# Kernel optimization log

Measured on AMD Instinct MI355X. Metric: run time of the kernel, lower is better.

## Reference

```python
import jax, jax.numpy as jnp
import numpy as np
import math

B, S, D, H = 4, 2048, 768, 12
DK = D // H

def setup_inputs() -> dict:
    key = jax.random.key(0)
    ks = jax.random.split(key, 12)
    sc = 1.0 / math.sqrt(D)
    return {
        'Q': jax.random.normal(ks[0], (B, S, D), jnp.float32),
        'K': jax.random.normal(ks[1], (B, S, D), jnp.float32),
        'V': jax.random.normal(ks[2], (B, S, D), jnp.float32),
        'mask': jax.random.randint(ks[3], (B, 1, S, S), 0, 2, jnp.int32),
        'Wq': jax.random.normal(ks[4], (D, D), jnp.float32) * sc,
        'bq': jnp.zeros((D,), jnp.float32),
        'Wk': jax.random.normal(ks[5], (D, D), jnp.float32) * sc,
        'bk': jnp.zeros((D,), jnp.float32),
        'Wv': jax.random.normal(ks[6], (D, D), jnp.float32) * sc,
        'bv': jnp.zeros((D,), jnp.float32),
        'Wo': jax.random.normal(ks[7], (D, D), jnp.float32) * sc,
        'bo': jnp.zeros((D,), jnp.float32),
    }

def _split_heads(x):
    # [B,S,D] -> [B,H,S,DK]
    return x.reshape(B, S, H, DK).transpose(0, 2, 1, 3)

def reference(Q, K, V, mask, Wq, bq, Wk, bk, Wv, bv, Wo, bo):
    q = _split_heads(Q @ Wq.T + bq)
    k = _split_heads(K @ Wk.T + bk)
    v = _split_heads(V @ Wv.T + bv)
    scores = jnp.einsum('bhqd,bhkd->bhqk', q, k) / math.sqrt(DK)
    # Faithful to the source: masked positions are filled with -1e-9 (NOT -inf)
    scores = jnp.where(mask == 0, jnp.float32(-1e-9), scores)
    attn = jax.nn.softmax(scores, axis=-1)
    x = jnp.einsum('bhqk,bhkd->bhqd', attn, v)          # [B,H,S,DK]
    x = x.transpose(0, 2, 1, 3).reshape(B, S, D)         # [B,S,D]
    return x @ Wo.T + bo
```

## Files before the change

kernel.cpp:

```cpp
#include <hip/hip_runtime.h>

#define BB 4
#define SS 2048
#define DD 768
#define HH 12
#define DKK 64
#define MM (BB*SS)

typedef __attribute__((ext_vector_type(8))) short bf16x8;
typedef __attribute__((ext_vector_type(4))) float f32x4;

#define GLDS(g, l) __builtin_amdgcn_global_load_lds( \
    (const __attribute__((address_space(1))) unsigned int*)(g), \
    (__attribute__((address_space(3))) unsigned int*)(l), 16, 0, 0)

__device__ __forceinline__ unsigned short f2bf(float f) {
    union { float f; unsigned int u; } v; v.f = f;
    unsigned int r = v.u + 0x7fffu + ((v.u >> 16) & 1u);
    return (unsigned short)(r >> 16);
}

__global__ void cvt_bf16(const float* __restrict__ src, unsigned short* __restrict__ dst, int n4) {
    int i = blockIdx.x * blockDim.x + threadIdx.x;
    if (i >= n4) return;
    float4 v = ((const float4*)src)[i];
    ushort4 o;
    o.x = f2bf(v.x); o.y = f2bf(v.y); o.z = f2bf(v.z); o.w = f2bf(v.w);
    ((ushort4*)dst)[i] = o;
}

__global__ void mask_pack(const int* __restrict__ mask, unsigned int* __restrict__ mbits) {
    int t = blockIdx.x * blockDim.x + threadIdx.x;
    int m = mask[t];
    unsigned long long b = __ballot(m != 0);
    int l = t & 63;
    if (l == 0)       mbits[t >> 5] = (unsigned int)b;
    else if (l == 32) mbits[t >> 5] = (unsigned int)(b >> 32);
}

__global__ __launch_bounds__(256) void gemm_qkv(
    const unsigned short* __restrict__ Qc, const unsigned short* __restrict__ Kc, const unsigned short* __restrict__ Vc,
    const unsigned short* __restrict__ Wq, const unsigned short* __restrict__ Wk, const unsigned short* __restrict__ Wv,
    const float* __restrict__ bq, const float* __restrict__ bk, const float* __restrict__ bv,
    unsigned short* __restrict__ qb, unsigned short* __restrict__ kb, unsigned short* __restrict__ vt)
{
    __shared__ unsigned short As[128*32];
    __shared__ unsigned short Bs[128*32];
    const int mat = blockIdx.z;
    const unsigned short* X = mat == 0 ? Qc : mat == 1 ? Kc : Vc;
    const unsigned short* W = mat == 0 ? Wq : mat == 1 ? Wk : Wv;
    const float* bias        = mat == 0 ? bq : mat == 1 ? bk : bv;

    const int tid  = threadIdx.x;
    const int lane = tid & 63;
    const int w    = tid >> 6;
    const int wm   = w >> 1, wn = w & 1;
    const int quad = lane >> 4, c = lane & 15;
    const int m0 = blockIdx.y * 128, n0 = blockIdx.x * 128;

    f32x4 acc[4][4];
    #pragma unroll
    for (int i = 0; i < 4; i++)
        #pragma unroll
        for (int j = 0; j < 4; j++) acc[i][j] = (f32x4){0.f, 0.f, 0.f, 0.f};

    const int ch0 = tid, ch1 = 256 + tid;
    const int r0 = ch0 >> 2, cc0 = (ch0 & 3) << 3;
    const int r1 = ch1 >> 2, cc1 = (ch1 & 3) << 3;
    const unsigned short* Xg0 = X + (size_t)(m0 + r0) * DD + cc0;
    const unsigned short* Xg1 = X + (size_t)(m0 + r1) * DD + cc1;
    const unsigned short* Wg0 = W + (size_t)(n0 + r0) * DD + cc0;
    const unsigned short* Wg1 = W + (size_t)(n0 + r1) * DD + cc1;

    for (int k0 = 0; k0 < DD; k0 += 32) {
        GLDS(Xg0 + k0, As + ch0 * 8);
        GLDS(Xg1 + k0, As + ch1 * 8);
        GLDS(Wg0 + k0, Bs + ch0 * 8);
        GLDS(Wg1 + k0, Bs + ch1 * 8);
        __syncthreads();
        bf16x8 a[4], b[4];
        #pragma unroll
        for (int t = 0; t < 4; t++) {
            a[t] = *(const bf16x8*)(As + ((wm * 64 + t * 16 + c) * 32 + quad * 8));
            b[t] = *(const bf16x8*)(Bs + ((wn * 64 + t * 16 + c) * 32 + quad * 8));
        }
        #pragma unroll
        for (int tm = 0; tm < 4; tm++)
            #pragma unroll
            for (int tn = 0; tn < 4; tn++)
                acc[tm][tn] = __builtin_amdgcn_mfma_f32_16x16x32_bf16(a[tm], b[tn], acc[tm][tn], 0, 0, 0);
        __syncthreads();
    }

    if (mat < 2) {
        unsigned short* out = mat == 0 ? qb : kb;
        #pragma unroll
        for (int tn = 0; tn < 4; tn++) {
            const int col = n0 + wn * 64 + tn * 16 + c;
            const float bz = bias[col];
            #pragma unroll
            for (int tm = 0; tm < 4; tm++) {
                const int row = m0 + wm * 64 + tm * 16 + quad * 4;
                #pragma unroll
                for (int r = 0; r < 4; r++)
                    out[(size_t)(row + r) * DD + col] = f2bf(acc[tm][tn][r] + bz);
            }
        }
    } else {
        #pragma unroll
        for (int tn = 0; tn < 4; tn++) {
            const int col = n0 + wn * 64 + tn * 16 + c;
            const float bz = bias[col];
            const int h = col >> 6, dk = col & 63;
            #pragma unroll
            for (int tm = 0; tm < 4; tm++) {
                const int row = m0 + wm * 64 + tm * 16 + quad * 4;
                const int bb = row >> 11, s = row & 2047;
                ushort4 pk;
                pk.x = f2bf(acc[tm][tn][0] + bz);
                pk.y = f2bf(acc[tm][tn][1] + bz);
                pk.z = f2bf(acc[tm][tn][2] + bz);
                pk.w = f2bf(acc[tm][tn][3] + bz);
                *(ushort4*)(vt + ((((size_t)bb * HH + h) * DKK + dk) * SS + s)) = pk;
            }
        }
    }
}

#define EXPSCALE 0.18033688011112042f

__global__ __launch_bounds__(256, 6) void flash(
    const unsigned short* __restrict__ qb, const unsigned short* __restrict__ kb,
    const unsigned short* __restrict__ vt, const unsigned int* __restrict__ mbits,
    unsigned short* __restrict__ ob)
{
    __shared__ unsigned short Ks[2][64*32];
    __shared__ unsigned short Vs[2][64*32];
    __shared__ unsigned short Pb[4][16][72];

    const int bh = blockIdx.y;
    const int bi = bh / HH, h = bh % HH;
    const int tid  = threadIdx.x;
    const int w    = tid >> 6, lane = tid & 63;
    const int quad = lane >> 4, c = lane & 15;
    const int q0 = blockIdx.x * 64 + w * 16;

    const unsigned short* qbase = qb + (size_t)(bi * SS + q0 + c) * DD + h * DKK + quad * 8;
    const bf16x8 qa0 = *(const bf16x8*)(qbase);
    const bf16x8 qa1 = *(const bf16x8*)(qbase + 32);

    const int sr = tid >> 2, sc8 = (tid & 3) << 3;
    const unsigned short* kg0 = kb + ((size_t)bi * SS + sr) * DD + h * DKK + sc8;
    const unsigned short* vg0 = vt + (((size_t)bi * HH + h) * DKK + sr) * SS + sc8;
    unsigned short* lk0 = Ks[0] + tid * 8;
    unsigned short* lk1 = Ks[1] + tid * 8;
    unsigned short* lv0 = Vs[0] + tid * 8;
    unsigned short* lv1 = Vs[1] + tid * 8;

    const unsigned int* mrow = mbits + (size_t)(bi * SS + q0 + c) * (SS / 32);

    f32x4 o[4];
    #pragma unroll
    for (int i = 0; i < 4; i++) o[i] = (f32x4){0.f, 0.f, 0.f, 0.f};
    float rs = 0.f;

    for (int k0 = 0; k0 < SS; k0 += 64) {
        const unsigned short* kg = kg0 + (size_t)k0 * DD;
        const unsigned short* vg = vg0 + k0;
        GLDS(kg,      lk0);
        GLDS(kg + 32, lk1);
        GLDS(vg,      lv0);
        GLDS(vg + 32, lv1);
        __syncthreads();

        const uint2 mw = *(const uint2*)(mrow + (k0 >> 5));
        const unsigned long long mm =
            (((unsigned long long)mw.y << 32) | mw.x) >> (quad * 4);

        #pragma unroll
        for (int nt = 0; nt < 4; nt++) {
            const bf16x8 kf0 = *(const bf16x8*)(Ks[0] + (nt * 16 + c) * 32 + quad * 8);
            const bf16x8 kf1 = *(const bf16x8*)(Ks[1] + (nt * 16 + c) * 32 + quad * 8);
            f32x4 st = (f32x4){0.f, 0.f, 0.f, 0.f};
            st = __builtin_amdgcn_mfma_f32_16x16x32_bf16(kf0, qa0, st, 0, 0, 0);
            st = __builtin_amdgcn_mfma_f32_16x16x32_bf16(kf1, qa1, st, 0, 0, 0);
            const unsigned int mb = (unsigned int)(mm >> (nt * 16));
            unsigned int pk[2];
            #pragma unroll
            for (int r2 = 0; r2 < 2; r2++) {
                float sv0 = st[r2 * 2]     * EXPSCALE;
                float sv1 = st[r2 * 2 + 1] * EXPSCALE;
                sv0 = (mb & (1u << (r2 * 2)))     ? sv0 : 0.0f;
                sv1 = (mb & (1u << (r2 * 2 + 1))) ? sv1 : 0.0f;
                const float p0 = __builtin_amdgcn_exp2f(sv0);
                const float p1 = __builtin_amdgcn_exp2f(sv1);
                rs += p0 + p1;
                union { float f; unsigned int u; } u0, u1; u0.f = p0; u1.f = p1;
                pk[r2] = __builtin_amdgcn_perm(u1.u + 0x8000u, u0.u + 0x8000u, 0x07060302);
            }
            *(uint2*)(&Pb[w][c][nt * 16 + quad * 4]) = make_uint2(pk[0], pk[1]);
        }

        const bf16x8 pa0 = *(const bf16x8*)(&Pb[w][c][quad * 8]);
        const bf16x8 pa1 = *(const bf16x8*)(&Pb[w][c][32 + quad * 8]);
        #pragma unroll
        for (int nt = 0; nt < 4; nt++) {
            const bf16x8 vf0 = *(const bf16x8*)(Vs[0] + (nt * 16 + c) * 32 + quad * 8);
            const bf16x8 vf1 = *(const bf16x8*)(Vs[1] + (nt * 16 + c) * 32 + quad * 8);
            o[nt] = __builtin_amdgcn_mfma_f32_16x16x32_bf16(pa0, vf0, o[nt], 0, 0, 0);
            o[nt] = __builtin_amdgcn_mfma_f32_16x16x32_bf16(pa1, vf1, o[nt], 0, 0, 0);
        }
        __syncthreads();
    }

    rs += __shfl_xor(rs, 16);
    rs += __shfl_xor(rs, 32);
    const float rn = __builtin_amdgcn_rcpf(rs);
    float rr[4];
    #pragma unroll
    for (int reg = 0; reg < 4; reg++)
        rr[reg] = __shfl(rn, quad * 4 + reg, 64);

    unsigned short* op = ob + (size_t)(bi * SS + q0 + quad * 4) * DD + h * DKK + c;
    #pragma unroll
    for (int nt = 0; nt < 4; nt++)
        #pragma unroll
        for (int reg = 0; reg < 4; reg++)
            op[(size_t)reg * DD + nt * 16] = f2bf(o[nt][reg] * rr[reg]);
}

__global__ __launch_bounds__(256) void gemm_out(
    const unsigned short* __restrict__ A, const unsigned short* __restrict__ W,
    const float* __restrict__ bias, float* __restrict__ out)
{
    __shared__ unsigned short As[128*32];
    __shared__ unsigned short Bs[128*32];
    const int tid  = threadIdx.x;
    const int lane = tid & 63;
    const int w    = tid >> 6;
    const int wm   = w >> 1, wn = w & 1;
    const int quad = lane >> 4, c = lane & 15;
    const int m0 = blockIdx.y * 128, n0 = blockIdx.x * 128;

    f32x4 acc[4][4];
    #pragma unroll
    for (int i = 0; i < 4; i++)
        #pragma unroll
        for (int j = 0; j < 4; j++) acc[i][j] = (f32x4){0.f, 0.f, 0.f, 0.f};

    const int ch0 = tid, ch1 = 256 + tid;
    const int r0 = ch0 >> 2, cc0 = (ch0 & 3) << 3;
    const int r1 = ch1 >> 2, cc1 = (ch1 & 3) << 3;
    const unsigned short* Ag0 = A + (size_t)(m0 + r0) * DD + cc0;
    const unsigned short* Ag1 = A + (size_t)(m0 + r1) * DD + cc1;
    const unsigned short* Wg0 = W + (size_t)(n0 + r0) * DD + cc0;
    const unsigned short* Wg1 = W + (size_t)(n0 + r1) * DD + cc1;

    for (int k0 = 0; k0 < DD; k0 += 32) {
        GLDS(Ag0 + k0, As + ch0 * 8);
        GLDS(Ag1 + k0, As + ch1 * 8);
        GLDS(Wg0 + k0, Bs + ch0 * 8);
        GLDS(Wg1 + k0, Bs + ch1 * 8);
        __syncthreads();
        bf16x8 a[4], b[4];
        #pragma unroll
        for (int t = 0; t < 4; t++) {
            a[t] = *(const bf16x8*)(As + ((wm * 64 + t * 16 + c) * 32 + quad * 8));
            b[t] = *(const bf16x8*)(Bs + ((wn * 64 + t * 16 + c) * 32 + quad * 8));
        }
        #pragma unroll
        for (int tm = 0; tm < 4; tm++)
            #pragma unroll
            for (int tn = 0; tn < 4; tn++)
                acc[tm][tn] = __builtin_amdgcn_mfma_f32_16x16x32_bf16(a[tm], b[tn], acc[tm][tn], 0, 0, 0);
        __syncthreads();
    }

    #pragma unroll
    for (int tn = 0; tn < 4; tn++) {
        const int col = n0 + wn * 64 + tn * 16 + c;
        const float bz = bias[col];
        #pragma unroll
        for (int tm = 0; tm < 4; tm++) {
            const int row = m0 + wm * 64 + tm * 16 + quad * 4;
            #pragma unroll
            for (int r = 0; r < 4; r++)
                out[(size_t)(row + r) * DD + col] = acc[tm][tn][r] + bz;
        }
    }
}

extern "C" void kernel_launch(void* const* d_in, const int* in_sizes, int n_in,
                              void* d_out, int out_size, void* d_ws, size_t ws_size,
                              hipStream_t stream) {
    (void)in_sizes; (void)n_in; (void)out_size; (void)ws_size;
    const float* Q    = (const float*)d_in[0];
    const float* K    = (const float*)d_in[1];
    const float* V    = (const float*)d_in[2];
    const int*   mask = (const int*)d_in[3];
    const float* Wq   = (const float*)d_in[4];
    const float* bq   = (const float*)d_in[5];
    const float* Wk   = (const float*)d_in[6];
    const float* bk   = (const float*)d_in[7];
    const float* Wv   = (const float*)d_in[8];
    const float* bv   = (const float*)d_in[9];
    const float* Wo   = (const float*)d_in[10];
    const float* bo   = (const float*)d_in[11];
    float* out = (float*)d_out;

    char* ws = (char*)d_ws;
    size_t off = 0;
    auto alloc = [&](size_t bytes) { char* p = ws + off; off += (bytes + 255) & ~255ULL; return p; };
    const size_t act = (size_t)MM * DD * 2;
    unsigned short* Qc  = (unsigned short*)alloc(act);
    unsigned short* Kc  = (unsigned short*)alloc(act);
    unsigned short* Vc  = (unsigned short*)alloc(act);
    unsigned short* Wqc = (unsigned short*)alloc((size_t)DD * DD * 2);
    unsigned short* Wkc = (unsigned short*)alloc((size_t)DD * DD * 2);
    unsigned short* Wvc = (unsigned short*)alloc((size_t)DD * DD * 2);
    unsigned short* Woc = (unsigned short*)alloc((size_t)DD * DD * 2);
    unsigned short* qb  = (unsigned short*)alloc(act);
    unsigned short* kb  = (unsigned short*)alloc(act);
    unsigned short* vt  = (unsigned short*)alloc(act);
    unsigned int*  mbits = (unsigned int*)alloc((size_t)BB * SS * (SS / 32) * 4);
    unsigned short* ob = Qc;

    const int nact4 = MM * DD / 4;
    const int nw4   = DD * DD / 4;
    cvt_bf16<<<dim3(nact4 / 256), 256, 0, stream>>>(Q, Qc, nact4);
    cvt_bf16<<<dim3(nact4 / 256), 256, 0, stream>>>(K, Kc, nact4);
    cvt_bf16<<<dim3(nact4 / 256), 256, 0, stream>>>(V, Vc, nact4);
    cvt_bf16<<<dim3(nw4 / 256),   256, 0, stream>>>(Wq, Wqc, nw4);
    cvt_bf16<<<dim3(nw4 / 256),   256, 0, stream>>>(Wk, Wkc, nw4);
    cvt_bf16<<<dim3(nw4 / 256),   256, 0, stream>>>(Wv, Wvc, nw4);
    cvt_bf16<<<dim3(nw4 / 256),   256, 0, stream>>>(Wo, Woc, nw4);
    mask_pack<<<dim3(BB * SS * SS / 256), 256, 0, stream>>>(mask, mbits);
    gemm_qkv<<<dim3(DD / 128, MM / 128, 3), 256, 0, stream>>>(
        Qc, Kc, Vc, Wqc, Wkc, Wvc, bq, bk, bv, qb, kb, vt);
    flash<<<dim3(SS / 64, BB * HH), 256, 0, stream>>>(qb, kb, vt, mbits, ob);
    gemm_out<<<dim3(DD / 128, MM / 128), 256, 0, stream>>>(ob, Woc, bo, out);
}
```

Before: 389.8 us.

## Fuse prep kernels, double-buffer and swizzle flash tiles, two query tiles per wave

The eight conversion and mask-packing launches become one prep kernel, which removes launch overhead. The flash kernel now handles 128 queries per block, two 16-row tiles per wave, so each K/V tile in LDS is reused twice. It also double-buffers the K/V loads so the next tile is fetched during compute, dropping one barrier per iteration, and XOR-swizzles the LDS columns to avoid bank conflicts. In exchange it uses more registers and LDS (occupancy hint lowered from 6 to 3) and launches half as many flash blocks.

After: 374.0 us. -4.0%, faster.

```diff
diff --git a/kernel.cpp b/kernel.cpp
--- a/kernel.cpp
+++ b/kernel.cpp
@@ -20,22 +20,48 @@
     return (unsigned short)(r >> 16);
 }
 
-__global__ void cvt_bf16(const float* __restrict__ src, unsigned short* __restrict__ dst, int n4) {
-    int i = blockIdx.x * blockDim.x + threadIdx.x;
-    if (i >= n4) return;
-    float4 v = ((const float4*)src)[i];
-    ushort4 o;
-    o.x = f2bf(v.x); o.y = f2bf(v.y); o.z = f2bf(v.z); o.w = f2bf(v.w);
-    ((ushort4*)dst)[i] = o;
-}
-
-__global__ void mask_pack(const int* __restrict__ mask, unsigned int* __restrict__ mbits) {
-    int t = blockIdx.x * blockDim.x + threadIdx.x;
-    int m = mask[t];
-    unsigned long long b = __ballot(m != 0);
-    int l = t & 63;
-    if (l == 0)       mbits[t >> 5] = (unsigned int)b;
-    else if (l == 32) mbits[t >> 5] = (unsigned int)(b >> 32);
+#define NACT4 (MM*DD/4)
+#define ABLK  (NACT4/256)
+#define NW4   (DD*DD/4)
+#define WBLK  (NW4/256)
+#define MBLK  (BB*SS*SS/256)
+
+__global__ void prep(
+    const float* __restrict__ Q, const float* __restrict__ K, const float* __restrict__ V,
+    const float* __restrict__ Wq, const float* __restrict__ Wk, const float* __restrict__ Wv,
+    const float* __restrict__ Wo, const int* __restrict__ mask,
+    unsigned short* __restrict__ Qc, unsigned short* __restrict__ Kc, unsigned short* __restrict__ Vc,
+    unsigned short* __restrict__ Wqc, unsigned short* __restrict__ Wkc, unsigned short* __restrict__ Wvc,
+    unsigned short* __restrict__ Woc, unsigned int* __restrict__ mbits)
+{
+    const int bx = blockIdx.x;
+    if (bx < 3 * ABLK) {
+        const int seg = bx / ABLK;
+        const float* s = seg == 0 ? Q : seg == 1 ? K : V;
+        unsigned short* d = seg == 0 ? Qc : seg == 1 ? Kc : Vc;
+        const int i = (bx - seg * ABLK) * 256 + threadIdx.x;
+        float4 v = ((const float4*)s)[i];
+        ushort4 o;
+        o.x = f2bf(v.x); o.y = f2bf(v.y); o.z = f2bf(v.z); o.w = f2bf(v.w);
+        ((ushort4*)d)[i] = o;
+    } else if (bx < 3 * ABLK + 4 * WBLK) {
+        const int b2 = bx - 3 * ABLK;
+        const int seg = b2 / WBLK;
+        const float* s = seg == 0 ? Wq : seg == 1 ? Wk : seg == 2 ? Wv : Wo;
+        unsigned short* d = seg == 0 ? Wqc : seg == 1 ? Wkc : seg == 2 ? Wvc : Woc;
+        const int i = (b2 - seg * WBLK) * 256 + threadIdx.x;
+        float4 v = ((const float4*)s)[i];
+        ushort4 o;
+        o.x = f2bf(v.x); o.y = f2bf(v.y); o.z = f2bf(v.z); o.w = f2bf(v.w);
+        ((ushort4*)d)[i] = o;
+    } else {
+        const int t = (bx - (3 * ABLK + 4 * WBLK)) * 256 + threadIdx.x;
+        const int m = mask[t];
+        unsigned long long b = __ballot(m != 0);
+        const int l = t & 63;
+        if (l == 0)       mbits[t >> 5] = (unsigned int)b;
+        else if (l == 32) mbits[t >> 5] = (unsigned int)(b >> 32);
+    }
 }
 
 __global__ __launch_bounds__(256) void gemm_qkv(
@@ -129,104 +155,140 @@
 
 #define EXPSCALE 0.18033688011112042f
 
-__global__ __launch_bounds__(256, 6) void flash(
+__global__ __launch_bounds__(256, 3) void flash(
     const unsigned short* __restrict__ qb, const unsigned short* __restrict__ kb,
     const unsigned short* __restrict__ vt, const unsigned int* __restrict__ mbits,
     unsigned short* __restrict__ ob)
 {
-    __shared__ unsigned short Ks[2][64*32];
-    __shared__ unsigned short Vs[2][64*32];
-    __shared__ unsigned short Pb[4][16][72];
+    __shared__ unsigned short Ks[2][2][64*32];
+    __shared__ unsigned short Vs[2][2][64*32];
+    __shared__ unsigned short Pb[4][32][72];
 
     const int bh = blockIdx.y;
     const int bi = bh / HH, h = bh % HH;
     const int tid  = threadIdx.x;
     const int w    = tid >> 6, lane = tid & 63;
     const int quad = lane >> 4, c = lane & 15;
-    const int q0 = blockIdx.x * 64 + w * 16;
-
-    const unsigned short* qbase = qb + (size_t)(bi * SS + q0 + c) * DD + h * DKK + quad * 8;
-    const bf16x8 qa0 = *(const bf16x8*)(qbase);
-    const bf16x8 qa1 = *(const bf16x8*)(qbase + 32);
-
-    const int sr = tid >> 2, sc8 = (tid & 3) << 3;
-    const unsigned short* kg0 = kb + ((size_t)bi * SS + sr) * DD + h * DKK + sc8;
-    const unsigned short* vg0 = vt + (((size_t)bi * HH + h) * DKK + sr) * SS + sc8;
-    unsigned short* lk0 = Ks[0] + tid * 8;
-    unsigned short* lk1 = Ks[1] + tid * 8;
-    unsigned short* lv0 = Vs[0] + tid * 8;
-    unsigned short* lv1 = Vs[1] + tid * 8;
-
-    const unsigned int* mrow = mbits + (size_t)(bi * SS + q0 + c) * (SS / 32);
-
-    f32x4 o[4];
-    #pragma unroll
-    for (int i = 0; i < 4; i++) o[i] = (f32x4){0.f, 0.f, 0.f, 0.f};
-    float rs = 0.f;
-
-    for (int k0 = 0; k0 < SS; k0 += 64) {
-        const unsigned short* kg = kg0 + (size_t)k0 * DD;
-        const unsigned short* vg = vg0 + k0;
-        GLDS(kg,      lk0);
-        GLDS(kg + 32, lk1);
-        GLDS(vg,      lv0);
-        GLDS(vg + 32, lv1);
-        __syncthreads();
-
-        const uint2 mw = *(const uint2*)(mrow + (k0 >> 5));
-        const unsigned long long mm =
-            (((unsigned long long)mw.y << 32) | mw.x) >> (quad * 4);
+    const int q0w = blockIdx.x * 128 + w * 32;
+
+    bf16x8 qa[2][2];
+    #pragma unroll
+    for (int mt = 0; mt < 2; mt++) {
+        const unsigned short* qbase = qb + (size_t)(bi * SS + q0w + mt * 16 + c) * DD + h * DKK + quad * 8;
+        qa[mt][0] = *(const bf16x8*)(qbase);
+        qa[mt][1] = *(const bf16x8*)(qbase + 32);
+    }
+
+    const int sr = tid >> 2, slot = tid & 3;
+    const int lc = ((slot ^ (sr & 3)) << 3);
+    const unsigned short* kgb = kb + ((size_t)bi * SS + sr) * DD + h * DKK + lc;
+    const unsigned short* vgb = vt + (((size_t)bi * HH + h) * DKK + sr) * SS + lc;
+    unsigned short* lds_k0[2] = { Ks[0][0] + tid * 8, Ks[1][0] + tid * 8 };
+    unsigned short* lds_k1[2] = { Ks[0][1] + tid * 8, Ks[1][1] + tid * 8 };
+    unsigned short* lds_v0[2] = { Vs[0][0] + tid * 8, Vs[1][0] + tid * 8 };
+    unsigned short* lds_v1[2] = { Vs[0][1] + tid * 8, Vs[1][1] + tid * 8 };
+
+    const unsigned int* mrow0 = mbits + (size_t)(bi * SS + q0w + c) * (SS / 32);
+    const unsigned int* mrow1 = mrow0 + (size_t)16 * (SS / 32);
+
+    f32x4 o[2][4];
+    #pragma unroll
+    for (int mt = 0; mt < 2; mt++)
+        #pragma unroll
+        for (int nt = 0; nt < 4; nt++) o[mt][nt] = (f32x4){0.f, 0.f, 0.f, 0.f};
+    float rs[2] = {0.f, 0.f};
+
+    const int sw = ((quad ^ (c & 3)) << 3);
+
+    GLDS(kgb,      lds_k0[0]);
+    GLDS(kgb + 32, lds_k1[0]);
+    GLDS(vgb,      lds_v0[0]);
+    GLDS(vgb + 32, lds_v1[0]);
+
+    for (int t = 0; t < SS / 64; t++) {
+        const int k0 = t * 64, par = t & 1;
+        __syncthreads();
+        if (t < SS / 64 - 1) {
+            const unsigned short* kg = kgb + (size_t)(k0 + 64) * DD;
+            const unsigned short* vg = vgb + (k0 + 64);
+            GLDS(kg,      lds_k0[par ^ 1]);
+            GLDS(kg + 32, lds_k1[par ^ 1]);
+            GLDS(vg,      lds_v0[par ^ 1]);
+            GLDS(vg + 32, lds_v1[par ^ 1]);
+        }
+
+        const uint2 mw0 = *(const uint2*)(mrow0 + (k0 >> 5));
+        const uint2 mw1 = *(const uint2*)(mrow1 + (k0 >> 5));
+        const unsigned long long mm[2] = {
+            ((((unsigned long long)mw0.y << 32) | mw0.x) >> (quad * 4)),
+            ((((unsigned long long)mw1.y << 32) | mw1.x) >> (quad * 4)) };
 
         #pragma unroll
         for (int nt = 0; nt < 4; nt++) {
-            const bf16x8 kf0 = *(const bf16x8*)(Ks[0] + (nt * 16 + c) * 32 + quad * 8);
-            const bf16x8 kf1 = *(const bf16x8*)(Ks[1] + (nt * 16 + c) * 32 + quad * 8);
-            f32x4 st = (f32x4){0.f, 0.f, 0.f, 0.f};
-            st = __builtin_amdgcn_mfma_f32_16x16x32_bf16(kf0, qa0, st, 0, 0, 0);
-            st = __builtin_amdgcn_mfma_f32_16x16x32_bf16(kf1, qa1, st, 0, 0, 0);
-            const unsigned int mb = (unsigned int)(mm >> (nt * 16));
-            unsigned int pk[2];
-            #pragma unroll
-            for (int r2 = 0; r2 < 2; r2++) {
-                float sv0 = st[r2 * 2]     * EXPSCALE;
-                float sv1 = st[r2 * 2 + 1] * EXPSCALE;
-                sv0 = (mb & (1u << (r2 * 2)))     ? sv0 : 0.0f;
-                sv1 = (mb & (1u << (r2 * 2 + 1))) ? sv1 : 0.0f;
-                const float p0 = __builtin_amdgcn_exp2f(sv0);
-                const float p1 = __builtin_amdgcn_exp2f(sv1);
-                rs += p0 + p1;
-                union { float f; unsigned int u; } u0, u1; u0.f = p0; u1.f = p1;
-                pk[r2] = __builtin_amdgcn_perm(u1.u + 0x8000u, u0.u + 0x8000u, 0x07060302);
+            const bf16x8 kf0 = *(const bf16x8*)(&Ks[par][0][(nt * 16 + c) * 32 + sw]);
+            const bf16x8 kf1 = *(const bf16x8*)(&Ks[par][1][(nt * 16 + c) * 32 + sw]);
+            #pragma unroll
+            for (int mt = 0; mt < 2; mt++) {
+                f32x4 st = (f32x4){0.f, 0.f, 0.f, 0.f};
+                st = __builtin_amdgcn_mfma_f32_16x16x32_bf16(kf0, qa[mt][0], st, 0, 0, 0);
+                st = __builtin_amdgcn_mfma_f32_16x16x32_bf16(kf1, qa[mt][1], st, 0, 0, 0);
+                const unsigned int mb = (unsigned int)(mm[mt] >> (nt * 16));
+                unsigned int pk[2];
+                #pragma unroll
+                for (int r2 = 0; r2 < 2; r2++) {
+                    float sv0 = st[r2 * 2]     * EXPSCALE;
+                    float sv1 = st[r2 * 2 + 1] * EXPSCALE;
+                    sv0 = (mb & (1u << (r2 * 2)))     ? sv0 : 0.0f;
+                    sv1 = (mb & (1u << (r2 * 2 + 1))) ? sv1 : 0.0f;
+                    const float p0 = __builtin_amdgcn_exp2f(sv0);
+                    const float p1 = __builtin_amdgcn_exp2f(sv1);
+                    rs[mt] += p0 + p1;
+                    union { float f; unsigned int u; } u0, u1; u0.f = p0; u1.f = p1;
+                    pk[r2] = __builtin_amdgcn_perm(u1.u + 0x8000u, u0.u + 0x8000u, 0x07060302);
+                }
+                *(uint2*)(&Pb[w][mt * 16 + c][nt * 16 + quad * 4]) = make_uint2(pk[0], pk[1]);
             }
-            *(uint2*)(&Pb[w][c][nt * 16 + quad * 4]) = make_uint2(pk[0], pk[1]);
-        }
-
-        const bf16x8 pa0 = *(const bf16x8*)(&Pb[w][c][quad * 8]);
-        const bf16x8 pa1 = *(const bf16x8*)(&Pb[w][c][32 + quad * 8]);
+        }
+
+        bf16x8 pa[2][2];
+        #pragma unroll
+        for (int mt = 0; mt < 2; mt++) {
+            pa[mt][0] = *(const bf16x8*)(&Pb[w][mt * 16 + c][quad * 8]);
+            pa[mt][1] = *(const bf16x8*)(&Pb[w][mt * 16 + c][32 + quad * 8]);
+        }
         #pragma unroll
         for (int nt = 0; nt < 4; nt++) {
-            const bf16x8 vf0 = *(const bf16x8*)(Vs[0] + (nt * 16 + c) * 32 + quad * 8);
-            const bf16x8 vf1 = *(const bf16x8*)(Vs[1] + (nt * 16 + c) * 32 + quad * 8);
-            o[nt] = __builtin_amdgcn_mfma_f32_16x16x32_bf16(pa0, vf0, o[nt], 0, 0, 0);
-            o[nt] = __builtin_amdgcn_mfma_f32_16x16x32_bf16(pa1, vf1, o[nt], 0, 0, 0);
-        }
-        __syncthreads();
-    }
-
-    rs += __shfl_xor(rs, 16);
-    rs += __shfl_xor(rs, 32);
-    const float rn = __builtin_amdgcn_rcpf(rs);
-    float rr[4];
-    #pragma unroll
-    for (int reg = 0; reg < 4; reg++)
-        rr[reg] = __shfl(rn, quad * 4 + reg, 64);
-
-    unsigned short* op = ob + (size_t)(bi * SS + q0 + quad * 4) * DD + h * DKK + c;
-    #pragma unroll
-    for (int nt = 0; nt < 4; nt++)
+            const bf16x8 vf0 = *(const bf16x8*)(&Vs[par][0][(nt * 16 + c) * 32 + sw]);
+            const bf16x8 vf1 = *(const bf16x8*)(&Vs[par][1][(nt * 16 + c) * 32 + sw]);
+            #pragma unroll
+            for (int mt = 0; mt < 2; mt++) {
+                o[mt][nt] = __builtin_amdgcn_mfma_f32_16x16x32_bf16(pa[mt][0], vf0, o[mt][nt], 0, 0, 0);
+                o[mt][nt] = __builtin_amdgcn_mfma_f32_16x16x32_bf16(pa[mt][1], vf1, o[mt][nt], 0, 0, 0);
+            }
+        }
+    }
+
+    float rr[2][4];
+    #pragma unroll
+    for (int mt = 0; mt < 2; mt++) {
+        float v = rs[mt];
+        v += __shfl_xor(v, 16);
+        v += __shfl_xor(v, 32);
+        const float rn = __builtin_amdgcn_rcpf(v);
         #pragma unroll
         for (int reg = 0; reg < 4; reg++)
-            op[(size_t)reg * DD + nt * 16] = f2bf(o[nt][reg] * rr[reg]);
+            rr[mt][reg] = __shfl(rn, quad * 4 + reg, 64);
+    }
+
+    #pragma unroll
+    for (int mt = 0; mt < 2; mt++) {
+        unsigned short* op = ob + (size_t)(bi * SS + q0w + mt * 16 + quad * 4) * DD + h * DKK + c;
+        #pragma unroll
+        for (int nt = 0; nt < 4; nt++)
+            #pragma unroll
+            for (int reg = 0; reg < 4; reg++)
+                op[(size_t)reg * DD + nt * 16] = f2bf(o[mt][nt][reg] * rr[mt][reg]);
+    }
 }
 
 __global__ __launch_bounds__(256) void gemm_out(
@@ -325,18 +387,10 @@
     unsigned int*  mbits = (unsigned int*)alloc((size_t)BB * SS * (SS / 32) * 4);
     unsigned short* ob = Qc;
 
-    const int nact4 = MM * DD / 4;
-    const int nw4   = DD * DD / 4;
-    cvt_bf16<<<dim3(nact4 / 256), 256, 0, stream>>>(Q, Qc, nact4);
-    cvt_bf16<<<dim3(nact4 / 256), 256, 0, stream>>>(K, Kc, nact4);
-    cvt_bf16<<<dim3(nact4 / 256), 256, 0, stream>>>(V, Vc, nact4);
-    cvt_bf16<<<dim3(nw4 / 256),   256, 0, stream>>>(Wq, Wqc, nw4);
-    cvt_bf16<<<dim3(nw4 / 256),   256, 0, stream>>>(Wk, Wkc, nw4);
-    cvt_bf16<<<dim3(nw4 / 256),   256, 0, stream>>>(Wv, Wvc, nw4);
-    cvt_bf16<<<dim3(nw4 / 256),   256, 0, stream>>>(Wo, Woc, nw4);
-    mask_pack<<<dim3(BB * SS * SS / 256), 256, 0, stream>>>(mask, mbits);
+    prep<<<dim3(3 * ABLK + 4 * WBLK + MBLK), 256, 0, stream>>>(
+        Q, K, V, Wq, Wk, Wv, Wo, mask, Qc, Kc, Vc, Wqc, Wkc, Wvc, Woc, mbits);
     gemm_qkv<<<dim3(DD / 128, MM / 128, 3), 256, 0, stream>>>(
         Qc, Kc, Vc, Wqc, Wkc, Wvc, bq, bk, bv, qb, kb, vt);
-    flash<<<dim3(SS / 64, BB * HH), 256, 0, stream>>>(qb, kb, vt, mbits, ob);
+    flash<<<dim3(SS / 128, BB * HH), 256, 0, stream>>>(qb, kb, vt, mbits, ob);
     gemm_out<<<dim3(DD / 128, MM / 128), 256, 0, stream>>>(ob, Woc, bo, out);
 }
```
